# Kernel optimization log

Measured on AMD Instinct MI355X. Metric: run time of the kernel, lower is better.

The kernel has to match this reference:

```python
import jax, jax.numpy as jnp
import numpy as np

B, T, NODE, IN_CH = 4, 8192, 64, 3
F, L, OUT, H = 256, 10, 48, 4
SFI_LAYER = (1, 3, 5, 7)
S = len(SFI_LAYER)
ALPHA = 1.0
EPS = 1e-5


def setup_inputs():
    ks = iter(jax.random.split(jax.random.key(0), 40))
    def nrm(shape, s=0.02):
        return jax.random.normal(next(ks), shape, jnp.float32) * s
    return {
        "x": jax.random.normal(next(ks), (B, IN_CH, T, NODE), jnp.float32),
        "mask": jnp.ones((B, 1, T), jnp.float32),
        "conv_in_w": nrm((S + 1, IN_CH)), "conv_in_b": nrm((S + 1,)),
        "conv_t_w": nrm((F, NODE)), "conv_t_b": nrm((F,)),
        "sfi_cs_w": nrm((S, F, NODE)), "sfi_cs_b": nrm((S, F)),
        "sfi_ff1_w": nrm((S, F, F)), "sfi_ff1_b": nrm((S, F)),
        "sfi_ff2_w": nrm((S, F, F)), "sfi_ff2_b": nrm((S, F)),
        "ff_w": nrm((L, F, F, 3)), "ff_b": nrm((L, F)),
        "qw": nrm((L, F, F)), "qb": nrm((L, F)),
        "kw": nrm((L, F, F)), "kb": nrm((L, F)),
        "vw": nrm((L, F, F)), "vb": nrm((L, F)),
        "ow": nrm((L, F, F)), "ob": nrm((L, F)),
        "co_w": nrm((L, F, F)), "co_b": nrm((L, F)),
        "out_w": nrm((OUT, F)), "out_b": nrm((OUT,)),
    }


def _dconv1d(x, w, b, dilation):
    # x: [B,C,T], w: [O,I,3]; 'same' length via padding=dilation
    y = jax.lax.conv_general_dilated(
        x, w, window_strides=(1,), padding=[(dilation, dilation)],
        rhs_dilation=(dilation,), dimension_numbers=("NCH", "OIH", "NCH"))
    return y + b[None, :, None]


def _inorm(x):
    # InstanceNorm1d, affine=False: normalize each (b,c) over T, biased var
    m = x.mean(-1, keepdims=True)
    v = x.var(-1, keepdims=True)
    return (x - m) * jax.lax.rsqrt(v + EPS)


def _lin_att(q, wq, bq, wk, bk, wv, bv, wo, bo, mask):
    # q: [B,L,C]; sigmoid-kernelized linear attention
    Bn, Ln, C = q.shape
    d = C // H
    def heads(w, b):
        return (q @ w.T + b).reshape(Bn, Ln, H, d).transpose(0, 2, 1, 3)
    Q = jax.nn.sigmoid(heads(wq, bq))  # [B,H,L,d]
    K = jax.nn.sigmoid(heads(wk, bk))
    V = heads(wv, bv)
    KV = jnp.einsum("bhsd,bhse->bhde", K, V)               # [B,H,d,d]
    Z = 1.0 / jnp.einsum("bhld,bhd->bhl", Q, K.sum(2) + 1e-6)
    o = jnp.einsum("bhde,bhld,bhl->bhle", KV, Q, Z)         # [B,H,L,d]
    o = o.transpose(0, 2, 1, 3).reshape(Bn, Ln, C) @ wo.T + bo
    return o * mask[:, 0, :, None]


def _sfi(fs, ft, csw, csb, f1w, f1b, f2w, f2b, mask):
    # fs: [B,T,node], ft: [B,F,T]
    fsc = jnp.einsum("btn,fn->bft", fs, csw) + csb[None, :, None]
    attn = jax.nn.softmax(jnp.einsum("bct,bdt->bcd", fsc, ft) / ft.shape[-1], axis=-1)
    cross = jnp.einsum("bcd,bdt->bct", attn, ft) + ft
    h = cross.transpose(0, 2, 1)                           # [B,T,F]
    h = jax.nn.gelu(h @ f1w.T + f1b, approximate=False) @ f2w.T + f2b
    return (h.transpose(0, 2, 1) + ft) * mask


def _att_module(x, ffw, ffb, wq, bq, wk, bk, wv, bv, wo, bo, cow, cob, mask, dilation):
    out = jax.nn.relu(_dconv1d(x, ffw, ffb, dilation))
    qn = _inorm(out).transpose(0, 2, 1)                    # [B,T,F]
    out = ALPHA * _lin_att(qn, wq, bq, wk, bk, wv, bv, wo, bo, mask).transpose(0, 2, 1) + out
    out = jnp.einsum("bct,oc->bot", out, cow) + cob[None, :, None]
    return (x + out) * mask


def reference(x, mask, conv_in_w, conv_in_b, conv_t_w, conv_t_b,
              sfi_cs_w, sfi_cs_b, sfi_ff1_w, sfi_ff1_b, sfi_ff2_w, sfi_ff2_b,
              ff_w, ff_b, qw, qb, kw, kb, vw, vb, ow, ob, co_w, co_b,
              out_w, out_b):
    # eval mode: all dropouts are identity
    xi = jnp.einsum("bitn,oi->botn", x, conv_in_w) + conv_in_b[None, :, None, None]
    feature_s = xi[:, :S]                                  # [B,S,T,node]
    ft = xi[:, S].transpose(0, 2, 1)                       # [B,node,T]
    fst = jnp.einsum("bnt,fn->bft", ft, conv_t_w) + conv_t_b[None, :, None]
    count = 0
    for i in range(L):
        if i in SFI_LAYER:
            fst = _sfi(feature_s[:, count], fst,
                       sfi_cs_w[count], sfi_cs_b[count],
                       sfi_ff1_w[count], sfi_ff1_b[count],
                       sfi_ff2_w[count], sfi_ff2_b[count], mask)
            count += 1
        fst = _att_module(fst, ff_w[i], ff_b[i], qw[i], qb[i], kw[i], kb[i],
                          vw[i], vb[i], ow[i], ob[i], co_w[i], co_b[i], mask, 2 ** i)
    out = jnp.einsum("bct,oc->bot", fst, out_w) + out_b[None, :, None]
    return out * mask
```

## Files before the change

kernel.cpp:

```cpp
#include <hip/hip_runtime.h>

#define T_ 8192
#define B_ 4

typedef _Float16 h16;
typedef _Float16 half8 __attribute__((ext_vector_type(8)));
typedef float    f32x4 __attribute__((ext_vector_type(4)));

__device__ __forceinline__ void split2(float v, h16* hp, h16* lp) {
  h16 h = (h16)v; *hp = h; *lp = (h16)(v - (float)h);
}
__device__ __forceinline__ float join2(h16 h, h16 l) {
  return (float)h + (float)l;
}
__device__ __forceinline__ void gl2lds16(const void* g, void* l) {
  __builtin_amdgcn_global_load_lds(
      (const __attribute__((address_space(1))) unsigned int*)g,
      (__attribute__((address_space(3))) unsigned int*)l, 16, 0, 0);
}

__global__ __launch_bounds__(256) void init_fs_k(
    const float* __restrict__ x, const float* __restrict__ cw,
    const float* __restrict__ cb, h16* __restrict__ sh, h16* __restrict__ sl,
    int c)
{
  size_t idx = (size_t)blockIdx.x * 256 + threadIdx.x;
  int n = (int)(idx & 63);
  int t = (int)((idx >> 6) & (T_ - 1));
  int b = (int)(idx >> 19);
  float x0 = x[(((size_t)b*3 + 0)*T_ + t)*64 + n];
  float x1 = x[(((size_t)b*3 + 1)*T_ + t)*64 + n];
  float x2 = x[(((size_t)b*3 + 2)*T_ + t)*64 + n];
  float v = cb[c] + x0*cw[c*3] + x1*cw[c*3+1] + x2*cw[c*3+2];
  split2(v, &sh[idx], &sl[idx]);
}

__global__ __launch_bounds__(256) void wsplit_k(
    const float* __restrict__ src, h16* __restrict__ dh, h16* __restrict__ dl,
    int n)
{
  int i = blockIdx.x*256 + threadIdx.x;
  if (i < n) split2(src[i], &dh[i], &dl[i]);
}

__global__ __launch_bounds__(256) void wsplit_out_k(
    const float* __restrict__ src, h16* __restrict__ dh, h16* __restrict__ dl)
{
  int i = blockIdx.x*256 + threadIdx.x;
  int row = i >> 8;
  float v = (row < 48) ? src[i] : 0.f;
  split2(v, &dh[i], &dl[i]);
}

__global__ __launch_bounds__(256) void prep_layer_k(
    const float* __restrict__ ffw, const float* __restrict__ cow,
    const float* __restrict__ ow, const float* __restrict__ ob,
    const float* __restrict__ cob,
    h16* __restrict__ dh,
    float* __restrict__ bias3, float* __restrict__ stats)
{
  int blk = blockIdx.x, tid = threadIdx.x;
  if (blk < 1024) {
    int i = blk*256 + tid;
    if (i < 196608) {
      int tap = i >> 16, nk = i & 65535;
      dh[i] = (h16)ffw[(size_t)nk*3 + tap];
    } else {
      int e = i - 196608;
      int n = e >> 8, k = e & 255;
      dh[196608 + n*512 + 256 + k] = (h16)cow[e];
    }
  } else if (blk < 1280) {
    int n = blk - 1024;
    __shared__ float Ar[256];
    int k = tid;
    Ar[k] = cow[n*256 + k];
    __syncthreads();
    float acc = 0.f;
    #pragma unroll 4
    for (int j = 0; j < 256; ++j) acc = fmaf(Ar[j], ow[j*256 + k], acc);
    dh[196608 + n*512 + k] = (h16)acc;
  } else if (blk == 1280) {
    int n = tid;
    float s = cob[n];
    #pragma unroll 4
    for (int j = 0; j < 256; ++j) s = fmaf(cow[n*256 + j], ob[j], s);
    bias3[n] = s;
  } else {
    stats[(blk - 1281)*256 + tid] = 0.f;
  }
}

__global__ __launch_bounds__(256) void sprep_k(
    const float* __restrict__ f1, const float* __restrict__ f2,
    const float* __restrict__ cs, h16* __restrict__ dh, h16* __restrict__ dl)
{
  int i = blockIdx.x*256 + threadIdx.x;
  float v = (i < 65536) ? f1[i] : (i < 131072) ? f2[i-65536] : cs[i-131072];
  split2(v, &dh[i], &dl[i]);
}

__global__ __launch_bounds__(256) void nwnb_k(
    const float* __restrict__ qw, const float* __restrict__ kw,
    const float* __restrict__ vw,
    const float* __restrict__ qb, const float* __restrict__ kb,
    const float* __restrict__ vb,
    const float* __restrict__ stats,
    h16* __restrict__ dh, float* __restrict__ bias2)
{
  int blk = blockIdx.x, tid = threadIdx.x;
  if (blk < 3072) {
    int i = blk*256 + tid;
    int k = i & 255;
    int b = (i >> 16) & 3;
    int sel = i >> 18;
    float sm = stats[b*512 + k] * (1.f/T_);
    float s2 = stats[b*512 + 256 + k] * (1.f/T_);
    float iv = rsqrtf(fmaxf(s2 - sm*sm, 0.f) + 1e-5f);
    const float* w = sel == 0 ? kw : sel == 1 ? vw : qw;
    dh[i] = (h16)(w[i & 65535] * iv);
  } else {
    int base = (blk - 3072) * 4;
    int g = tid >> 6, l = tid & 63;
    int id = base + g;
    int n = id & 255, b = (id >> 8) & 3, sel = id >> 10;
    const float* w  = sel == 0 ? kw : sel == 1 ? vw : qw;
    const float* bb = sel == 0 ? kb : sel == 1 ? vb : qb;
    float s = 0.f;
    #pragma unroll
    for (int j = 0; j < 4; ++j) {
      int k = l*4 + j;
      float sm = stats[b*512 + k] * (1.f/T_);
      float s2 = stats[b*512 + 256 + k] * (1.f/T_);
      float iv = rsqrtf(fmaxf(s2 - sm*sm, 0.f) + 1e-5f);
      s += sm * iv * w[n*256 + k];
    }
    #pragma unroll
    for (int off = 32; off > 0; off >>= 1) s += __shfl_xor(s, off);
    if (l == 0) bias2[id] = bb[n] - s;
  }
}

__global__ __launch_bounds__(256) void mmrow_k(
    const float* __restrict__ A, const float* __restrict__ Bm,
    h16* __restrict__ dh)
{
  int n  = blockIdx.x & 255;
  int bb = blockIdx.x >> 8;
  __shared__ float Ar[256];
  int k = threadIdx.x;
  Ar[k] = A[n*256 + k];
  __syncthreads();
  const float* Bb = Bm + (size_t)bb*65536;
  float acc = 0.f;
  #pragma unroll 4
  for (int j = 0; j < 256; ++j) acc = fmaf(Ar[j], Bb[j*256 + k], acc);
  acc += Ar[k];
  dh[(size_t)bb*65536 + (size_t)n*256 + k] = (h16)acc;
}

template<int ACT, int SGL>
__global__ __launch_bounds__(256, 2) void gemm_p(
    const h16* __restrict__ Agh, const h16* __restrict__ Agl,
    const h16* __restrict__ Wgh, const h16* __restrict__ Wgl,
    const float* __restrict__ bias,
    const h16* __restrict__ Rh, const h16* __restrict__ Rl,
    h16* __restrict__ Ch, h16* __restrict__ Cl,
    int K, size_t wbs)
{
  int b  = blockIdx.z;
  int n0 = blockIdx.x * 128;
  int t0 = blockIdx.y * 128;
  const h16* Ah_g = Agh + (size_t)b*T_*K;
  const h16* Al_g = Agl + (size_t)b*T_*K;
  const h16* Wh_g = Wgh + (size_t)b*wbs;
  const h16* Wl_g = Wgl + (size_t)b*wbs;
  __shared__ h16 S[16384];
  int tid = threadIdx.x, l = tid & 63, wid = tid >> 6;
  int wr = wid >> 1, wc = wid & 1, lr = l & 15, kg = l >> 4;
  f32x4 acc[4][4];
  #pragma unroll
  for (int m = 0; m < 4; ++m)
    #pragma unroll
    for (int n = 0; n < 4; ++n) acc[m][n] = (f32x4){0.f,0.f,0.f,0.f};

  for (int k0 = 0; k0 < K; k0 += 32) {
    #pragma unroll
    for (int i = 0; i < 8; ++i) {
      int c = i*256 + tid;
      int p = c >> 9, r = (c >> 2) & 127, kc = c & 3;
      int ks = k0 + ((kc ^ ((r >> 1) & 3)) << 3);
      const h16* src = (p == 0) ? Ah_g + (size_t)(t0 + r)*K + ks
                     : (p == 1) ? Al_g + (size_t)(t0 + r)*K + ks
                     : (p == 2) ? Wh_g + (size_t)(n0 + r)*K + ks
                                : Wl_g + (size_t)(n0 + r)*K + ks;
      gl2lds16(src, S + (size_t)c*8);
    }
    __syncthreads();
    half8 ah[4], al[4], wh[4], wl[4];
    #pragma unroll
    for (int m = 0; m < 4; ++m) {
      int row = wr*64 + m*16 + lr;
      int ko = (kg ^ ((row >> 1) & 3)) * 8;
      ah[m] = *(const half8*)&S[row*32 + ko];
      al[m] = *(const half8*)&S[4096 + row*32 + ko];
    }
    #pragma unroll
    for (int n = 0; n < 4; ++n) {
      int row = wc*64 + n*16 + lr;
      int ko = (kg ^ ((row >> 1) & 3)) * 8;
      wh[n] = *(const half8*)&S[8192 + row*32 + ko];
      wl[n] = *(const half8*)&S[12288 + row*32 + ko];
    }
    #pragma unroll
    for (int m = 0; m < 4; ++m)
      #pragma unroll
      for (int n = 0; n < 4; ++n) {
        acc[m][n] = __builtin_amdgcn_mfma_f32_16x16x32_f16(ah[m], wh[n], acc[m][n], 0, 0, 0);
        acc[m][n] = __builtin_amdgcn_mfma_f32_16x16x32_f16(al[m], wh[n], acc[m][n], 0, 0, 0);
        acc[m][n] = __builtin_amdgcn_mfma_f32_16x16x32_f16(ah[m], wl[n], acc[m][n], 0, 0, 0);
      }
    __syncthreads();
  }
  float* Sf = (float*)S;
  const int LS = 132;
  int erow = tid >> 3;
  int ecol = (tid & 7) * 16;
  #pragma unroll
  for (int m = 0; m < 4; ++m) {
    int lr0 = wr*16 + kg*4;
    #pragma unroll
    for (int n = 0; n < 4; ++n) {
      int lcol = wc*64 + n*16 + lr;
      Sf[(lr0+0)*LS + lcol] = acc[m][n][0];
      Sf[(lr0+1)*LS + lcol] = acc[m][n][1];
      Sf[(lr0+2)*LS + lcol] = acc[m][n][2];
      Sf[(lr0+3)*LS + lcol] = acc[m][n][3];
    }
    __syncthreads();
    int grow = t0 + (erow >> 4)*64 + m*16 + (erow & 15);
    size_t off = ((size_t)b*T_ + grow)*256 + n0 + ecol;
    float f[16];
    #pragma unroll
    for (int j = 0; j < 16; ++j) f[j] = Sf[erow*LS + ecol + j];
    #pragma unroll
    for (int j = 0; j < 16; ++j) {
      float v = f[j];
      if (bias) v += bias[n0 + ecol + j];
      if (ACT == 1) v = fmaxf(v, 0.f);
      if (ACT == 2) v = 1.f/(1.f + __expf(-v));
      if (ACT == 3) v = 0.5f*v*(1.f + erff(v*0.7071067811865475f));
      f[j] = v;
    }
    if (Rh) {
      half8 rh0 = *(const half8*)(Rh + off), rh1 = *(const half8*)(Rh + off + 8);
      half8 rl0 = *(const half8*)(Rl + off), rl1 = *(const half8*)(Rl + off + 8);
      #pragma unroll
      for (int j = 0; j < 8; ++j) { f[j] += join2(rh0[j], rl0[j]); f[j+8] += join2(rh1[j], rl1[j]); }
    }
    if (SGL) {
      half8 o0, o1;
      #pragma unroll
      for (int j = 0; j < 8; ++j) { o0[j] = (h16)f[j]; o1[j] = (h16)f[j+8]; }
      *(half8*)(Ch + off) = o0; *(half8*)(Ch + off + 8) = o1;
    } else {
      half8 oh0, ol0, oh1, ol1;
      #pragma unroll
      for (int j = 0; j < 8; ++j) {
        h16 hh = (h16)f[j];   oh0[j] = hh; ol0[j] = (h16)(f[j]   - (float)hh);
        h16 h2 = (h16)f[j+8]; oh1[j] = h2; ol1[j] = (h16)(f[j+8] - (float)h2);
      }
      *(half8*)(Ch + off) = oh0; *(half8*)(Ch + off + 8) = oh1;
      *(half8*)(Cl + off) = ol0; *(half8*)(Cl + off + 8) = ol1;
    }
    __syncthreads();
  }
}

template<int ACT>
__global__ __launch_bounds__(256, 2) void gemm_p_wh(
    const h16* __restrict__ Agh, const h16* __restrict__ Agl,
    const h16* __restrict__ Wg,
    const float* __restrict__ bias,
    const h16* __restrict__ Rh, const h16* __restrict__ Rl,
    h16* __restrict__ Ch, h16* __restrict__ Cl,
    size_t wbs)
{
  int b  = blockIdx.z;
  int n0 = blockIdx.x * 128;
  int t0 = blockIdx.y * 128;
  const h16* Ah_g = Agh + (size_t)b*T_*256;
  const h16* Al_g = Agl + (size_t)b*T_*256;
  const h16* W_g  = Wg + (size_t)b*wbs;
  __shared__ h16 S[24576];
  int tid = threadIdx.x, l = tid & 63, wid = tid >> 6;
  int wr = wid >> 1, wc = wid & 1, lr = l & 15, kg = l >> 4;
  f32x4 acc[4][4];
  #pragma unroll
  for (int m = 0; m < 4; ++m)
    #pragma unroll
    for (int n = 0; n < 4; ++n) acc[m][n] = (f32x4){0.f,0.f,0.f,0.f};

  for (int k0 = 0; k0 < 256; k0 += 64) {
    #pragma unroll
    for (int i = 0; i < 12; ++i) {
      int c = i*256 + tid;
      int p = c >> 9, r = (c >> 2) & 127, kc = c & 3;
      int ks = k0 + (p & 1)*32 + ((kc ^ ((r >> 1) & 3)) << 3);
      const h16* src = (p < 2) ? Ah_g + (size_t)(t0 + r)*256 + ks
                     : (p < 4) ? Al_g + (size_t)(t0 + r)*256 + ks
                               : W_g  + (size_t)(n0 + r)*256 + ks;
      gl2lds16(src, S + (size_t)c*8);
    }
    __syncthreads();
    half8 a0[4], a1[4], l0[4], l1[4], w0[4], w1[4];
    #pragma unroll
    for (int m = 0; m < 4; ++m) {
      int row = wr*64 + m*16 + lr;
      int ko = (kg ^ ((row >> 1) & 3)) * 8;
      a0[m] = *(const half8*)&S[row*32 + ko];
      a1[m] = *(const half8*)&S[4096 + row*32 + ko];
      l0[m] = *(const half8*)&S[8192 + row*32 + ko];
      l1[m] = *(const half8*)&S[12288 + row*32 + ko];
    }
    #pragma unroll
    for (int n = 0; n < 4; ++n) {
      int row = wc*64 + n*16 + lr;
      int ko = (kg ^ ((row >> 1) & 3)) * 8;
      w0[n] = *(const half8*)&S[16384 + row*32 + ko];
      w1[n] = *(const half8*)&S[20480 + row*32 + ko];
    }
    #pragma unroll
    for (int m = 0; m < 4; ++m)
      #pragma unroll
      for (int n = 0; n < 4; ++n) {
        acc[m][n] = __builtin_amdgcn_mfma_f32_16x16x32_f16(a0[m], w0[n], acc[m][n], 0, 0, 0);
        acc[m][n] = __builtin_amdgcn_mfma_f32_16x16x32_f16(l0[m], w0[n], acc[m][n], 0, 0, 0);
        acc[m][n] = __builtin_amdgcn_mfma_f32_16x16x32_f16(a1[m], w1[n], acc[m][n], 0, 0, 0);
        acc[m][n] = __builtin_amdgcn_mfma_f32_16x16x32_f16(l1[m], w1[n], acc[m][n], 0, 0, 0);
      }
    __syncthreads();
  }
  float* Sf = (float*)S;
  const int LS = 132;
  int erow = tid >> 3;
  int ecol = (tid & 7) * 16;
  #pragma unroll
  for (int m = 0; m < 4; ++m) {
    int lr0 = wr*16 + kg*4;
    #pragma unroll
    for (int n = 0; n < 4; ++n) {
      int lcol = wc*64 + n*16 + lr;
      Sf[(lr0+0)*LS + lcol] = acc[m][n][0];
      Sf[(lr0+1)*LS + lcol] = acc[m][n][1];
      Sf[(lr0+2)*LS + lcol] = acc[m][n][2];
      Sf[(lr0+3)*LS + lcol] = acc[m][n][3];
    }
    __syncthreads();
    int grow = t0 + (erow >> 4)*64 + m*16 + (erow & 15);
    size_t off = ((size_t)b*T_ + grow)*256 + n0 + ecol;
    float f[16];
    #pragma unroll
    for (int j = 0; j < 16; ++j) {
      float v = Sf[erow*LS + ecol + j] + bias[n0 + ecol + j];
      if (ACT == 3) v = 0.5f*v*(1.f + erff(v*0.7071067811865475f));
      f[j] = v;
    }
    if (Rh) {
      half8 rh0 = *(const half8*)(Rh + off), rh1 = *(const half8*)(Rh + off + 8);
      half8 rl0 = *(const half8*)(Rl + off), rl1 = *(const half8*)(Rl + off + 8);
      #pragma unroll
      for (int j = 0; j < 8; ++j) { f[j] += join2(rh0[j], rl0[j]); f[j+8] += join2(rh1[j], rl1[j]); }
    }
    half8 oh0, ol0, oh1, ol1;
    #pragma unroll
    for (int j = 0; j < 8; ++j) {
      h16 hh = (h16)f[j];   oh0[j] = hh; ol0[j] = (h16)(f[j]   - (float)hh);
      h16 h2 = (h16)f[j+8]; oh1[j] = h2; ol1[j] = (h16)(f[j+8] - (float)h2);
    }
    *(half8*)(Ch + off) = oh0; *(half8*)(Ch + off + 8) = oh1;
    *(half8*)(Cl + off) = ol0; *(half8*)(Cl + off + 8) = ol1;
    __syncthreads();
  }
}

__global__ __launch_bounds__(256, 2) void gemm_attout(
    const h16* __restrict__ A1f, const h16* __restrict__ A2f,
    const h16* __restrict__ Wg,
    const float* __restrict__ bias,
    const h16* __restrict__ Rh, const h16* __restrict__ Rl,
    h16* __restrict__ Ch, h16* __restrict__ Cl)
{
  int b  = blockIdx.z;
  int n0 = blockIdx.x * 128;
  int t0 = blockIdx.y * 128;
  size_t abase = (size_t)b*T_*256;
  __shared__ h16 S[16384];
  int tid = threadIdx.x, l = tid & 63, wid = tid >> 6;
  int wr = wid >> 1, wc = wid & 1, lr = l & 15, kg = l >> 4;
  f32x4 acc[4][4];
  #pragma unroll
  for (int m = 0; m < 4; ++m)
    #pragma unroll
    for (int n = 0; n < 4; ++n) acc[m][n] = (f32x4){0.f,0.f,0.f,0.f};

  for (int k0 = 0; k0 < 512; k0 += 64) {
    #pragma unroll
    for (int i = 0; i < 8; ++i) {
      int c = i*256 + tid;
      int p = c >> 9, r = (c >> 2) & 127, kc = c & 3;
      int ks = k0 + (p & 1)*32 + ((kc ^ ((r >> 1) & 3)) << 3);
      const h16* src;
      if (p < 2) {
        if (ks < 256) src = A1f + abase + (size_t)(t0 + r)*256 + ks;
        else          src = A2f + abase + (size_t)(t0 + r)*256 + (ks - 256);
      } else {
        src = Wg + (size_t)(n0 + r)*512 + ks;
      }
      gl2lds16(src, S + (size_t)c*8);
    }
    __syncthreads();
    half8 a0[4], a1[4], w0[4], w1[4];
    #pragma unroll
    for (int m = 0; m < 4; ++m) {
      int row = wr*64 + m*16 + lr;
      int ko = (kg ^ ((row >> 1) & 3)) * 8;
      a0[m] = *(const half8*)&S[row*32 + ko];
      a1[m] = *(const half8*)&S[4096 + row*32 + ko];
    }
    #pragma unroll
    for (int n = 0; n < 4; ++n) {
      int row = wc*64 + n*16 + lr;
      int ko = (kg ^ ((row >> 1) & 3)) * 8;
      w0[n] = *(const half8*)&S[8192 + row*32 + ko];
      w1[n] = *(const half8*)&S[12288 + row*32 + ko];
    }
    #pragma unroll
    for (int m = 0; m < 4; ++m)
      #pragma unroll
      for (int n = 0; n < 4; ++n) {
        acc[m][n] = __builtin_amdgcn_mfma_f32_16x16x32_f16(a0[m], w0[n], acc[m][n], 0, 0, 0);
        acc[m][n] = __builtin_amdgcn_mfma_f32_16x16x32_f16(a1[m], w1[n], acc[m][n], 0, 0, 0);
      }
    __syncthreads();
  }
  float* Sf = (float*)S;
  const int LS = 132;
  int erow = tid >> 3;
  int ecol = (tid & 7) * 16;
  #pragma unroll
  for (int m = 0; m < 4; ++m) {
    int lr0 = wr*16 + kg*4;
    #pragma unroll
    for (int n = 0; n < 4; ++n) {
      int lcol = wc*64 + n*16 + lr;
      Sf[(lr0+0)*LS + lcol] = acc[m][n][0];
      Sf[(lr0+1)*LS + lcol] = acc[m][n][1];
      Sf[(lr0+2)*LS + lcol] = acc[m][n][2];
      Sf[(lr0+3)*LS + lcol] = acc[m][n][3];
    }
    __syncthreads();
    int grow = t0 + (erow >> 4)*64 + m*16 + (erow & 15);
    size_t off = ((size_t)b*T_ + grow)*256 + n0 + ecol;
    float f[16];
    #pragma unroll
    for (int j = 0; j < 16; ++j) f[j] = Sf[erow*LS + ecol + j] + bias[n0 + ecol + j];
    half8 rh0 = *(const half8*)(Rh + off), rh1 = *(const half8*)(Rh + off + 8);
    half8 rl0 = *(const half8*)(Rl + off), rl1 = *(const half8*)(Rl + off + 8);
    #pragma unroll
    for (int j = 0; j < 8; ++j) { f[j] += join2(rh0[j], rl0[j]); f[j+8] += join2(rh1[j], rl1[j]); }
    half8 oh0, ol0, oh1, ol1;
    #pragma unroll
    for (int j = 0; j < 8; ++j) {
      h16 hh = (h16)f[j];   oh0[j] = hh; ol0[j] = (h16)(f[j]   - (float)hh);
      h16 h2 = (h16)f[j+8]; oh1[j] = h2; ol1[j] = (h16)(f[j+8] - (float)h2);
    }
    *(half8*)(Ch + off) = oh0; *(half8*)(Ch + off + 8) = oh1;
    *(half8*)(Cl + off) = ol0; *(half8*)(Cl + off + 8) = ol1;
    __syncthreads();
  }
}

__global__ __launch_bounds__(256, 2) void gemm_qkv(
    const h16* __restrict__ Af, const h16* __restrict__ Wqkv,
    const float* __restrict__ bias2,
    h16* __restrict__ Kf, h16* __restrict__ Vf, h16* __restrict__ Qf)
{
  int fid = blockIdx.x;
  int swz = (fid & 7)*192 + (fid >> 3);
  int xsel = swz % 6;
  int sel = xsel >> 1;
  int n0  = (xsel & 1) * 128;
  int t0  = ((swz / 6) & 63) * 128;
  int b   = swz / 384;
  const h16* A_g = Af + (size_t)b*T_*256;
  const h16* W_g = Wqkv + (size_t)(sel*4 + b)*65536;
  const float* bias = bias2 + (size_t)(sel*4 + b)*256;
  h16* dst = sel == 0 ? Kf : sel == 1 ? Vf : Qf;
  __shared__ h16 S[16384];
  int tid = threadIdx.x, l = tid & 63, wid = tid >> 6;
  int wr = wid >> 1, wc = wid & 1, lr = l & 15, kg = l >> 4;
  f32x4 acc[4][4];
  #pragma unroll
  for (int m = 0; m < 4; ++m)
    #pragma unroll
    for (int n = 0; n < 4; ++n) acc[m][n] = (f32x4){0.f,0.f,0.f,0.f};

  for (int k0 = 0; k0 < 256; k0 += 64) {
    #pragma unroll
    for (int i = 0; i < 8; ++i) {
      int c = i*256 + tid;
      int p = c >> 9, r = (c >> 2) & 127, kc = c & 3;
      int ks = k0 + (p & 1)*32 + ((kc ^ ((r >> 1) & 3)) << 3);
      const h16* src = (p < 2) ? A_g + (size_t)(t0 + r)*256 + ks
                               : W_g + (size_t)(n0 + r)*256 + ks;
      gl2lds16(src, S + (size_t)c*8);
    }
    __syncthreads();
    half8 a0[4], a1[4], w0[4], w1[4];
    #pragma unroll
    for (int m = 0; m < 4; ++m) {
      int row = wr*64 + m*16 + lr;
      int ko = (kg ^ ((row >> 1) & 3)) * 8;
      a0[m] = *(const half8*)&S[row*32 + ko];
      a1[m] = *(const half8*)&S[4096 + row*32 + ko];
    }
    #pragma unroll
    for (int n = 0; n < 4; ++n) {
      int row = wc*64 + n*16 + lr;
      int ko = (kg ^ ((row >> 1) & 3)) * 8;
      w0[n] = *(const half8*)&S[8192 + row*32 + ko];
      w1[n] = *(const half8*)&S[12288 + row*32 + ko];
    }
    #pragma unroll
    for (int m = 0; m < 4; ++m)
      #pragma unroll
      for (int n = 0; n < 4; ++n) {
        acc[m][n] = __builtin_amdgcn_mfma_f32_16x16x32_f16(a0[m], w0[n], acc[m][n], 0, 0, 0);
        acc[m][n] = __builtin_amdgcn_mfma_f32_16x16x32_f16(a1[m], w1[n], acc[m][n], 0, 0, 0);
      }
    __syncthreads();
  }
  float* Sf = (float*)S;
  const int LS = 132;
  int erow = tid >> 3;
  int ecol = (tid & 7) * 16;
  #pragma unroll
  for (int m = 0; m < 4; ++m) {
    int lr0 = wr*16 + kg*4;
    #pragma unroll
    for (int n = 0; n < 4; ++n) {
      int lcol = wc*64 + n*16 + lr;
      Sf[(lr0+0)*LS + lcol] = acc[m][n][0];
      Sf[(lr0+1)*LS + lcol] = acc[m][n][1];
      Sf[(lr0+2)*LS + lcol] = acc[m][n][2];
      Sf[(lr0+3)*LS + lcol] = acc[m][n][3];
    }
    __syncthreads();
    int grow = t0 + (erow >> 4)*64 + m*16 + (erow & 15);
    size_t off = ((size_t)b*T_ + grow)*256 + n0 + ecol;
    half8 o0, o1;
    #pragma unroll
    for (int j = 0; j < 8; ++j) {
      float v0 = Sf[erow*LS + ecol + j]     + bias[n0 + ecol + j];
      float v1 = Sf[erow*LS + ecol + 8 + j] + bias[n0 + ecol + 8 + j];
      if (sel != 1) {
        v0 = 1.f/(1.f + __expf(-v0));
        v1 = 1.f/(1.f + __expf(-v1));
      }
      o0[j] = (h16)v0; o1[j] = (h16)v1;
    }
    *(half8*)(dst + off) = o0; *(half8*)(dst + off + 8) = o1;
    __syncthreads();
  }
}

__global__ __launch_bounds__(256, 2) void conv_p(
    const h16* __restrict__ Agh,
    const h16* __restrict__ Wg,
    const float* __restrict__ bias,
    h16* __restrict__ Cf,
    float* __restrict__ stats, const float* __restrict__ zbuf, int dil)
{
  int fid = blockIdx.x;
  int swz = (fid & 7)*64 + (fid >> 3);
  int n0 = (swz & 1) * 128;
  int t0 = ((swz >> 1) & 63) * 128;
  int b  = swz >> 7;
  const h16* Ah_g = Agh + (size_t)b*T_*256;
  __shared__ h16 S[16384];
  __shared__ float cstat[2][128];
  int tid = threadIdx.x, l = tid & 63, wid = tid >> 6;
  int wr = wid >> 1, wc = wid & 1, lr = l & 15, kg = l >> 4;
  f32x4 acc[4][4];
  #pragma unroll
  for (int m = 0; m < 4; ++m)
    #pragma unroll
    for (int n = 0; n < 4; ++n) acc[m][n] = (f32x4){0.f,0.f,0.f,0.f};

  for (int tap = 0; tap < 3; ++tap) {
    int off = (tap - 1) * dil;
    const h16* W_t = Wg + (size_t)tap*65536;
    for (int k0 = 0; k0 < 256; k0 += 64) {
      #pragma unroll
      for (int i = 0; i < 8; ++i) {
        int c = i*256 + tid;
        int p = c >> 9, r = (c >> 2) & 127, kc = c & 3;
        int ks = k0 + (p & 1)*32 + ((kc ^ ((r >> 1) & 3)) << 3);
        const h16* src;
        if (p < 2) {
          int rt = t0 + r + off;
          if ((unsigned)rt < (unsigned)T_)
            src = Ah_g + (size_t)rt*256 + ks;
          else
            src = (const h16*)zbuf;
        } else {
          src = W_t + (size_t)(n0 + r)*256 + ks;
        }
        gl2lds16(src, S + (size_t)c*8);
      }
      __syncthreads();
      half8 a0[4], a1[4], w0[4], w1[4];
      #pragma unroll
      for (int m = 0; m < 4; ++m) {
        int row = wr*64 + m*16 + lr;
        int ko = (kg ^ ((row >> 1) & 3)) * 8;
        a0[m] = *(const half8*)&S[row*32 + ko];
        a1[m] = *(const half8*)&S[4096 + row*32 + ko];
      }
      #pragma unroll
      for (int n = 0; n < 4; ++n) {
        int row = wc*64 + n*16 + lr;
        int ko = (kg ^ ((row >> 1) & 3)) * 8;
        w0[n] = *(const half8*)&S[8192 + row*32 + ko];
        w1[n] = *(const half8*)&S[12288 + row*32 + ko];
      }
      #pragma unroll
      for (int m = 0; m < 4; ++m)
        #pragma unroll
        for (int n = 0; n < 4; ++n) {
          acc[m][n] = __builtin_amdgcn_mfma_f32_16x16x32_f16(a0[m], w0[n], acc[m][n], 0, 0, 0);
          acc[m][n] = __builtin_amdgcn_mfma_f32_16x16x32_f16(a1[m], w1[n], acc[m][n], 0, 0, 0);
        }
      __syncthreads();
    }
  }
  cstat[tid >> 7][tid & 127] = 0.f;
  __syncthreads();
  #pragma unroll
  for (int n = 0; n < 4; ++n) {
    int cl = wc*64 + n*16 + lr;
    float bi = bias[n0 + cl];
    float s = 0.f, s2 = 0.f;
    #pragma unroll
    for (int m = 0; m < 4; ++m)
      #pragma unroll
      for (int r = 0; r < 4; ++r) {
        float v = fmaxf(acc[m][n][r] + bi, 0.f);
        acc[m][n][r] = v;
        s += v; s2 += v*v;
      }
    atomicAdd(&cstat[0][cl], s);
    atomicAdd(&cstat[1][cl], s2);
  }
  __syncthreads();
  if (tid < 128)      atomicAdd(&stats[b*512 + n0 + tid], cstat[0][tid]);
  else if (tid < 256) atomicAdd(&stats[b*512 + 256 + n0 + (tid-128)], cstat[1][tid-128]);
  __syncthreads();
  float* Sf = (float*)S;
  const int LS = 132;
  int erow = tid >> 3;
  int ecol = (tid & 7) * 16;
  #pragma unroll
  for (int m = 0; m < 4; ++m) {
    int lr0 = wr*16 + kg*4;
    #pragma unroll
    for (int n = 0; n < 4; ++n) {
      int lcol = wc*64 + n*16 + lr;
      Sf[(lr0+0)*LS + lcol] = acc[m][n][0];
      Sf[(lr0+1)*LS + lcol] = acc[m][n][1];
      Sf[(lr0+2)*LS + lcol] = acc[m][n][2];
      Sf[(lr0+3)*LS + lcol] = acc[m][n][3];
    }
    __syncthreads();
    int grow = t0 + (erow >> 4)*64 + m*16 + (erow & 15);
    size_t off2 = ((size_t)b*T_ + grow)*256 + n0 + ecol;
    half8 o0, o1;
    #pragma unroll
    for (int j = 0; j < 8; ++j) {
      o0[j] = (h16)Sf[erow*LS + ecol + j];
      o1[j] = (h16)Sf[erow*LS + ecol + 8 + j];
    }
    *(half8*)(Cf + off2) = o0; *(half8*)(Cf + off2 + 8) = o1;
    __syncthreads();
  }
}

__global__ __launch_bounds__(256) void kv_part_p(
    const h16* __restrict__ Kf, const h16* __restrict__ Vf,
    float* __restrict__ pkv)
{
  int bh = blockIdx.y, b = bh >> 2, h = bh & 3;
  int t0 = blockIdx.x * 512;
  __shared__ h16 S[2][64][64];
  __shared__ float ksum[64];
  int tid = threadIdx.x, l = tid & 63, wid = tid >> 6;
  int lr = l & 15, kg = l >> 4;
  if (tid < 64) ksum[tid] = 0.f;
  float ksp[8] = {};
  f32x4 acc[4];
  #pragma unroll
  for (int n = 0; n < 4; ++n) acc[n] = (f32x4){0.f,0.f,0.f,0.f};

  for (int k0 = 0; k0 < 512; k0 += 64) {
    __syncthreads();
    #pragma unroll
    for (int i = 0; i < 2; ++i) {
      int q = tid + i*256;
      int tt = q >> 3;
      int c8 = (q & 7) * 8;
      size_t row = ((size_t)b*T_ + t0 + k0 + tt)*256 + h*64;
      half8 k8 = *(const half8*)(Kf + row + c8);
      half8 v8 = *(const half8*)(Vf + row + c8);
      int ts = tt ^ ((q & 3) << 3);
      #pragma unroll
      for (int j = 0; j < 8; ++j) {
        S[0][c8+j][ts] = k8[j];
        S[1][c8+j][ts] = v8[j];
        ksp[j] += (float)k8[j];
      }
    }
    __syncthreads();
    half8 a0, a1, b0[4], b1[4];
    {
      int row = wid*16 + lr;
      int ko = (kg*8) ^ (((row >> 3) & 3) << 3);
      a0 = *(const half8*)&S[0][row][ko];
      a1 = *(const half8*)&S[0][row][32 + ko];
    }
    #pragma unroll
    for (int n = 0; n < 4; ++n) {
      int row = n*16 + lr;
      int ko = (kg*8) ^ (((row >> 3) & 3) << 3);
      b0[n] = *(const half8*)&S[1][row][ko];
      b1[n] = *(const half8*)&S[1][row][32 + ko];
    }
    #pragma unroll
    for (int n = 0; n < 4; ++n) {
      acc[n] = __builtin_amdgcn_mfma_f32_16x16x32_f16(a0, b0[n], acc[n], 0, 0, 0);
      acc[n] = __builtin_amdgcn_mfma_f32_16x16x32_f16(a1, b1[n], acc[n], 0, 0, 0);
    }
  }
  __syncthreads();
  {
    int dbase = (tid & 7) * 8;
    #pragma unroll
    for (int j = 0; j < 8; ++j) atomicAdd(&ksum[dbase + j], ksp[j]);
  }
  __syncthreads();
  float* dst = pkv + ((size_t)blockIdx.x*16 + bh)*4160;
  #pragma unroll
  for (int n = 0; n < 4; ++n) {
    int e = n*16 + lr;
    #pragma unroll
    for (int r = 0; r < 4; ++r) {
      int d = wid*16 + kg*4 + r;
      dst[d*64 + e] = acc[n][r];
    }
  }
  if (tid < 64) dst[4096 + tid] = ksum[tid];
}

__global__ __launch_bounds__(256) void kv_final_k(
    const float* __restrict__ pkv, float* __restrict__ kv)
{
  int bh = blockIdx.x;
  for (int idx = threadIdx.x; idx < 4160; idx += 256) {
    float s = 0.f;
    #pragma unroll
    for (int c = 0; c < 16; ++c) s += pkv[((size_t)c*16 + bh)*4160 + idx];
    kv[(size_t)bh*4160 + idx] = s;
  }
}

__global__ __launch_bounds__(256) void att_apply_p(
    const h16* __restrict__ Qf, const float* __restrict__ kv,
    h16* __restrict__ Of)
{
  int bh = blockIdx.y, b = bh >> 2, h = bh & 3;
  int t0 = blockIdx.x * 128;
  __shared__ float QsT[64][132];
  __shared__ float KVs[64][68];
  __shared__ float ks[64];
  int tid = threadIdx.x;
  const float* src = kv + (size_t)bh*4160;
  #pragma unroll
  for (int i = 0; i < 16; ++i) {
    int idx = tid + i*256;
    KVs[idx >> 6][idx & 63] = src[idx];
  }
  if (tid < 64) ks[tid] = src[4096 + tid] + 1e-6f;
  #pragma unroll
  for (int i = 0; i < 4; ++i) {
    int q8 = tid + i*256;
    int t  = q8 >> 3;
    int d8 = (q8 & 7) * 8;
    size_t off = ((size_t)b*T_ + t0 + t)*256 + h*64 + d8;
    half8 qh = *(const half8*)(Qf + off);
    #pragma unroll
    for (int j = 0; j < 8; ++j) QsT[d8+j][t] = (float)qh[j];
  }
  __syncthreads();
  int t2 = (tid >> 2) * 2;
  int e0 = (tid & 3) * 16;
  float acc[2][16] = {};
  float den[2] = {};
  for (int dd = 0; dd < 64; ++dd) {
    float2 q = *(const float2*)&QsT[dd][t2];
    float kd = ks[dd];
    den[0] = fmaf(q.x, kd, den[0]);
    den[1] = fmaf(q.y, kd, den[1]);
    float va[16];
    *(float4*)&va[0]  = *(const float4*)&KVs[dd][e0+0];
    *(float4*)&va[4]  = *(const float4*)&KVs[dd][e0+4];
    *(float4*)&va[8]  = *(const float4*)&KVs[dd][e0+8];
    *(float4*)&va[12] = *(const float4*)&KVs[dd][e0+12];
    #pragma unroll
    for (int j = 0; j < 16; ++j) {
      acc[0][j] = fmaf(q.x, va[j], acc[0][j]);
      acc[1][j] = fmaf(q.y, va[j], acc[1][j]);
    }
  }
  #pragma unroll
  for (int ti = 0; ti < 2; ++ti) {
    float z = 1.f / den[ti];
    size_t off = ((size_t)b*T_ + t0 + t2 + ti)*256 + h*64 + e0;
    half8 v0, v1;
    #pragma unroll
    for (int j = 0; j < 8; ++j) {
      v0[j] = (h16)(acc[ti][j] * z);
      v1[j] = (h16)(acc[ti][j+8] * z);
    }
    *(half8*)(Of + off) = v0;
    *(half8*)(Of + off + 8) = v1;
  }
}

__global__ __launch_bounds__(256, 2) void gram_part_p(
    const h16* __restrict__ Af, const h16* __restrict__ Bf,
    float* __restrict__ pg)
{
  int b = blockIdx.z;
  int quad = blockIdx.y;
  int slab = blockIdx.x;
  int c0 = (quad >> 1) * 128, d0 = (quad & 1) * 128;
  int t0 = slab * 256;
  __shared__ h16 S[2][128][64];
  int tid = threadIdx.x, l = tid & 63, wid = tid >> 6;
  int wr = wid >> 1, wc = wid & 1, lr = l & 15, kg = l >> 4;
  f32x4 acc[4][4];
  #pragma unroll
  for (int m = 0; m < 4; ++m)
    #pragma unroll
    for (int n = 0; n < 4; ++n) acc[m][n] = (f32x4){0.f,0.f,0.f,0.f};

  for (int k0 = 0; k0 < 256; k0 += 64) {
    #pragma unroll
    for (int i = 0; i < 4; ++i) {
      int q = tid + i*256;
      int tt = q >> 4;
      int c8 = (q & 15) * 8;
      size_t row = ((size_t)b*T_ + t0 + k0 + tt) * 256;
      half8 a8 = *(const half8*)(Af + row + c0 + c8);
      half8 b8 = *(const half8*)(Bf + row + d0 + c8);
      int ts = tt ^ ((q & 3) << 3);
      #pragma unroll
      for (int j = 0; j < 8; ++j) {
        S[0][c8+j][ts] = a8[j];
        S[1][c8+j][ts] = b8[j];
      }
    }
    __syncthreads();
    half8 a0[4], a1[4], b0[4], b1[4];
    #pragma unroll
    for (int m = 0; m < 4; ++m) {
      int row = wr*64 + m*16 + lr;
      int ko = (kg*8) ^ (((row >> 3) & 3) << 3);
      a0[m] = *(const half8*)&S[0][row][ko];
      a1[m] = *(const half8*)&S[0][row][32 + ko];
    }
    #pragma unroll
    for (int n = 0; n < 4; ++n) {
      int row = wc*64 + n*16 + lr;
      int ko = (kg*8) ^ (((row >> 3) & 3) << 3);
      b0[n] = *(const half8*)&S[1][row][ko];
      b1[n] = *(const half8*)&S[1][row][32 + ko];
    }
    #pragma unroll
    for (int m = 0; m < 4; ++m)
      #pragma unroll
      for (int n = 0; n < 4; ++n) {
        acc[m][n] = __builtin_amdgcn_mfma_f32_16x16x32_f16(a0[m], b0[n], acc[m][n], 0, 0, 0);
        acc[m][n] = __builtin_amdgcn_mfma_f32_16x16x32_f16(a1[m], b1[n], acc[m][n], 0, 0, 0);
      }
    __syncthreads();
  }
  float* dst = pg + ((size_t)(slab*B_ + b)*4 + quad)*16384;
  #pragma unroll
  for (int m = 0; m < 4; ++m)
    #pragma unroll
    for (int n = 0; n < 4; ++n) {
      int cl = wr*64 + m*16 + kg*4;
      int dl = wc*64 + n*16 + lr;
      #pragma unroll
      for (int r = 0; r < 4; ++r)
        dst[(size_t)(cl + r)*128 + dl] = acc[m][n][r];
    }
}

__global__ __launch_bounds__(64) void gram_smax_p(
    const float* __restrict__ pg, float* __restrict__ G)
{
  int row = blockIdx.x;
  int b = row >> 8, c = row & 255;
  int l = threadIdx.x;
  int d4 = l * 4;
  int quad = ((c >= 128) ? 2 : 0) | ((d4 >= 128) ? 1 : 0);
  size_t base = ((size_t)b*4 + quad)*16384 + (size_t)(c & 127)*128 + (d4 & 127);
  float s0 = 0.f, s1 = 0.f, s2 = 0.f, s3 = 0.f;
  for (int sl = 0; sl < 32; ++sl) {
    const float* p = pg + (size_t)sl*(B_*4*16384) + base;
    float4 v = *(const float4*)p;
    s0 += v.x; s1 += v.y; s2 += v.z; s3 += v.w;
  }
  float v[4] = {s0*(1.f/T_), s1*(1.f/T_), s2*(1.f/T_), s3*(1.f/T_)};
  float mx = fmaxf(fmaxf(v[0], v[1]), fmaxf(v[2], v[3]));
  #pragma unroll
  for (int off = 32; off > 0; off >>= 1) mx = fmaxf(mx, __shfl_xor(mx, off));
  float s = 0.f;
  #pragma unroll
  for (int j = 0; j < 4; ++j) { v[j] = __expf(v[j] - mx); s += v[j]; }
  #pragma unroll
  for (int off = 32; off > 0; off >>= 1) s += __shfl_xor(s, off);
  float inv = 1.f / s;
  float4 o = make_float4(v[0]*inv, v[1]*inv, v[2]*inv, v[3]*inv);
  *(float4*)(G + (size_t)b*65536 + (size_t)c*256 + d4) = o;
}

__global__ __launch_bounds__(256, 2) void gemm_out(
    const h16* __restrict__ Agh, const h16* __restrict__ Agl,
    const h16* __restrict__ Wgh, const h16* __restrict__ Wgl,
    const float* __restrict__ bn, const float* __restrict__ mask,
    float* __restrict__ out)
{
  int bt0 = blockIdx.x * 256;
  int b = bt0 >> 13;
  __shared__ h16 S[20480];
  int tid = threadIdx.x, l = tid & 63, wid = tid >> 6;
  int lr = l & 15, kg = l >> 4;
  f32x4 acc[4][4];
  #pragma unroll
  for (int m = 0; m < 4; ++m)
    #pragma unroll
    for (int n = 0; n < 4; ++n) acc[m][n] = (f32x4){0.f,0.f,0.f,0.f};

  for (int k0 = 0; k0 < 256; k0 += 32) {
    #pragma unroll
    for (int i = 0; i < 10; ++i) {
      int c = i*256 + tid;
      const h16* src;
      if (c < 2048) {
        int p = c >> 10, rem = c & 1023, r = rem >> 2, kc = rem & 3;
        int ks = k0 + ((kc ^ ((r >> 1) & 3)) << 3);
        src = (p ? Agl : Agh) + (size_t)(bt0 + r)*256 + ks;
      } else {
        int c2 = c - 2048;
        int p = c2 >> 8, rem = c2 & 255, r = rem >> 2, kc = rem & 3;
        int ks = k0 + ((kc ^ ((r >> 1) & 3)) << 3);
        src = (p ? Wgl : Wgh) + (size_t)r*256 + ks;
      }
      gl2lds16(src, S + (size_t)c*8);
    }
    __syncthreads();
    half8 ah[4], al[4], wh[4], wl[4];
    #pragma unroll
    for (int m = 0; m < 4; ++m) {
      int row = wid*64 + m*16 + lr;
      int ko = ((kg ^ ((row >> 1) & 3)) << 3);
      ah[m] = *(const half8*)&S[row*32 + ko];
      al[m] = *(const half8*)&S[8192 + row*32 + ko];
    }
    #pragma unroll
    for (int n = 0; n < 4; ++n) {
      int row = n*16 + lr;
      int ko = ((kg ^ ((row >> 1) & 3)) << 3);
      wh[n] = *(const half8*)&S[16384 + row*32 + ko];
      wl[n] = *(const half8*)&S[18432 + row*32 + ko];
    }
    #pragma unroll
    for (int m = 0; m < 4; ++m)
      #pragma unroll
      for (int n = 0; n < 4; ++n) {
        acc[m][n] = __builtin_amdgcn_mfma_f32_16x16x32_f16(ah[m], wh[n], acc[m][n], 0, 0, 0);
        acc[m][n] = __builtin_amdgcn_mfma_f32_16x16x32_f16(al[m], wh[n], acc[m][n], 0, 0, 0);
        acc[m][n] = __builtin_amdgcn_mfma_f32_16x16x32_f16(ah[m], wl[n], acc[m][n], 0, 0, 0);
      }
    __syncthreads();
  }
  #pragma unroll
  for (int m = 0; m < 4; ++m)
    #pragma unroll
    for (int n = 0; n < 4; ++n) {
      int col = n*16 + lr;
      if (col < 48) {
        float bi = bn[col];
        #pragma unroll
        for (int r = 0; r < 4; ++r) {
          int grow = bt0 + wid*64 + m*16 + kg*4 + r;
          int t = grow & (T_ - 1);
          out[((size_t)b*48 + col)*T_ + t] =
              (acc[m][n][r] + bi) * mask[(size_t)b*T_ + t];
        }
      }
    }
}

extern "C" void kernel_launch(void* const* d_in, const int* in_sizes, int n_in,
                              void* d_out, int out_size, void* d_ws, size_t ws_size,
                              hipStream_t stream) {
  const float* x         = (const float*)d_in[0];
  const float* mask      = (const float*)d_in[1];
  const float* conv_in_w = (const float*)d_in[2];
  const float* conv_in_b = (const float*)d_in[3];
  const float* conv_t_w  = (const float*)d_in[4];
  const float* conv_t_b  = (const float*)d_in[5];
  const float* sfi_cs_w  = (const float*)d_in[6];
  const float* sfi_cs_b  = (const float*)d_in[7];
  const float* sfi_ff1_w = (const float*)d_in[8];
  const float* sfi_ff1_b = (const float*)d_in[9];
  const float* sfi_ff2_w = (const float*)d_in[10];
  const float* sfi_ff2_b = (const float*)d_in[11];
  const float* ff_w      = (const float*)d_in[12];
  const float* ff_b      = (const float*)d_in[13];
  const float* qw = (const float*)d_in[14]; const float* qb = (const float*)d_in[15];
  const float* kw = (const float*)d_in[16]; const float* kb = (const float*)d_in[17];
  const float* vw = (const float*)d_in[18]; const float* vb = (const float*)d_in[19];
  const float* ow = (const float*)d_in[20]; const float* ob = (const float*)d_in[21];
  const float* co_w = (const float*)d_in[22]; const float* co_b = (const float*)d_in[23];
  const float* out_w = (const float*)d_in[24]; const float* out_b = (const float*)d_in[25];

  float* ws = (float*)d_ws;
  const size_t BT = (size_t)B_ * T_;
  const size_t NB = BT * 256;
  float* smallR = ws;
  float* bigR   = smallR + BT*64;
  float* GR     = bigR + 5*NB;
  float* statsR = GR + (size_t)B_*65536;
  float* kvR    = statsR + (size_t)B_*512;
  float* wsfiR  = kvR + 16*4160;
  float* zbufR  = wsfiR + 147456;

  h16* small_h = (h16*)smallR; h16* small_l = small_h + BT*64;
  h16 *bigH[5], *bigL[5];
  for (int i = 0; i < 5; ++i) { bigH[i] = (h16*)(bigR + (size_t)i*NB); bigL[i] = bigH[i] + NB; }
  float* Gf    = GR;
  float* stats = statsR;
  float* kvbuf = kvR;
  h16* wsfi_h = (h16*)wsfiR; h16* wsfi_l = wsfi_h + 147456;
  float* pkv   = smallR;
  h16* wqkv   = (h16*)smallR;
  h16* wf_h    = (h16*)smallR;
  h16* wlay   = (h16*)(smallR + 1064960);
  float* bias2 = smallR + 1392640;
  float* bias3 = smallR + 1395712;

  dim3 gh(2, T_/128, B_);
  dim3 b256(256);

  hipMemsetAsync(zbufR, 0, 64, stream);
  init_fs_k<<<dim3((unsigned)(BT*64/256)), b256, 0, stream>>>(x, conv_in_w, conv_in_b, small_h, small_l, 4);
  wsplit_k<<<dim3(64), b256, 0, stream>>>(conv_t_w, wsfi_h, wsfi_l, 16384);
  gemm_p<0,0><<<gh, b256, 0, stream>>>(small_h, small_l, wsfi_h, wsfi_l, conv_t_b,
                                       nullptr, nullptr, bigH[0], bigL[0], 64, 0);

  int ifst = 0;
  int fr[4] = {1, 2, 3, 4};
  int count = 0;
  for (int i = 0; i < 10; ++i) {
    if (i == 1 || i == 3 || i == 5 || i == 7) {
      int a = fr[0], bb = fr[1], c = fr[2], d = fr[3];
      sprep_k<<<dim3(576), b256, 0, stream>>>(sfi_ff1_w + (size_t)count*65536,
                                              sfi_ff2_w + (size_t)count*65536,
                                              sfi_cs_w + (size_t)count*16384,
                                              wsfi_h, wsfi_l);
      init_fs_k<<<dim3((unsigned)(BT*64/256)), b256, 0, stream>>>(x, conv_in_w, conv_in_b, small_h, small_l, count);
      gemm_p<0,1><<<gh, b256, 0, stream>>>(small_h, small_l, wsfi_h + 131072, wsfi_l + 131072,
                                           sfi_cs_b + count*256, nullptr, nullptr,
                                           bigH[a], nullptr, 64, 0);
      float* pgram = bigR + (size_t)bb*NB;
      gram_part_p<<<dim3(32, 4, B_), b256, 0, stream>>>(bigH[a], bigH[ifst], pgram);
      gram_smax_p<<<dim3(B_*256), dim3(64), 0, stream>>>(pgram, Gf);
      mmrow_k<<<dim3(B_*256), b256, 0, stream>>>(sfi_ff1_w + (size_t)count*65536, Gf, wf_h);
      gemm_p_wh<3><<<gh, b256, 0, stream>>>(bigH[ifst], bigL[ifst], wf_h,
                                            sfi_ff1_b + count*256, nullptr, nullptr,
                                            bigH[c], bigL[c], 65536);
      gemm_p_wh<0><<<gh, b256, 0, stream>>>(bigH[c], bigL[c], wsfi_h + 65536,
                                            sfi_ff2_b + count*256, bigH[ifst], bigL[ifst],
                                            bigH[d], bigL[d], 0);
      fr[0] = a; fr[1] = bb; fr[2] = c; fr[3] = ifst;
      ifst = d;
      ++count;
    }
    int a = fr[0], bb = fr[1], c = fr[2], d = fr[3];
    int dil = 1 << i;
    prep_layer_k<<<dim3(1289), b256, 0, stream>>>(ff_w + (size_t)i*196608,
                                                  co_w + (size_t)i*65536,
                                                  ow + (size_t)i*65536, ob + i*256,
                                                  co_b + i*256,
                                                  wlay, bias3, stats);
    conv_p<<<dim3(512), b256, 0, stream>>>(bigH[ifst], wlay, ff_b + i*256,
                                           bigH[a], stats, zbufR, dil);
    nwnb_k<<<dim3(3840), b256, 0, stream>>>(qw + (size_t)i*65536, kw + (size_t)i*65536,
                                            vw + (size_t)i*65536,
                                            qb + i*256, kb + i*256, vb + i*256,
                                            stats, wqkv, bias2);
    gemm_qkv<<<dim3(1536), b256, 0, stream>>>(bigH[a], wqkv, bias2,
                                              bigH[bb], bigH[c], bigH[d]);
    kv_part_p<<<dim3(16, 16), b256, 0, stream>>>(bigH[bb], bigH[c], pkv);
    kv_final_k<<<dim3(16), b256, 0, stream>>>(pkv, kvbuf);
    att_apply_p<<<dim3(T_/128, 16), b256, 0, stream>>>(bigH[d], kvbuf, bigH[d]);
    gemm_attout<<<gh, b256, 0, stream>>>(bigH[d], bigH[a],
                                         wlay + 196608, bias3,
                                         bigH[ifst], bigL[ifst], bigH[bb], bigL[bb]);
    fr[0] = a; fr[1] = c; fr[2] = d; fr[3] = ifst;
    ifst = bb;
  }
  wsplit_out_k<<<dim3(64), b256, 0, stream>>>(out_w, wsfi_h, wsfi_l);
  gemm_out<<<dim3((unsigned)(BT/256)), b256, 0, stream>>>(bigH[ifst], bigL[ifst], wsfi_h, wsfi_l,
                                                          out_b, mask, (float*)d_out);
}
```

Baseline: 1.945 ms.

## Move linear-attention apply onto MFMA with split-fp16 transposed KV

The attention-apply step now runs on fp16 MFMA instead of scalar fp32 FMA loops. KV is transposed and stored as hi/lo fp16 pairs, with the key-sum folded in as an extra column so the denominator comes out of the same matrix product. Q and KV tiles are loaded into swizzled LDS through direct global-to-LDS copies. This cuts ALU and LDS work in a kernel that runs every layer, but Q is used only in its fp16 form, and the output stores become scattered 2-byte writes.

```diff
diff --git a/kernel.cpp b/kernel.cpp
--- a/kernel.cpp
+++ b/kernel.cpp
@@ -772,77 +772,104 @@
 }
 
 __global__ __launch_bounds__(256) void kv_final_k(
-    const float* __restrict__ pkv, float* __restrict__ kv)
+    const float* __restrict__ pkv, h16* __restrict__ kvT)
 {
   int bh = blockIdx.x;
-  for (int idx = threadIdx.x; idx < 4160; idx += 256) {
+  for (int idx = threadIdx.x; idx < 5120; idx += 256) {
+    int e = idx >> 6, d = idx & 63;
     float s = 0.f;
-    #pragma unroll
-    for (int c = 0; c < 16; ++c) s += pkv[((size_t)c*16 + bh)*4160 + idx];
-    kv[(size_t)bh*4160 + idx] = s;
+    if (e < 64) {
+      #pragma unroll
+      for (int c = 0; c < 16; ++c) s += pkv[((size_t)c*16 + bh)*4160 + d*64 + e];
+    } else if (e == 64) {
+      #pragma unroll
+      for (int c = 0; c < 16; ++c) s += pkv[((size_t)c*16 + bh)*4160 + 4096 + d];
+      s += 1e-6f;
+    }
+    split2(s, &kvT[(size_t)bh*10240 + idx], &kvT[(size_t)bh*10240 + 5120 + idx]);
   }
 }
 
 __global__ __launch_bounds__(256) void att_apply_p(
-    const h16* __restrict__ Qf, const float* __restrict__ kv,
+    const h16* __restrict__ Qf, const h16* __restrict__ kvT,
     h16* __restrict__ Of)
 {
   int bh = blockIdx.y, b = bh >> 2, h = bh & 3;
   int t0 = blockIdx.x * 128;
-  __shared__ float QsT[64][132];
-  __shared__ float KVs[64][68];
-  __shared__ float ks[64];
-  int tid = threadIdx.x;
-  const float* src = kv + (size_t)bh*4160;
-  #pragma unroll
-  for (int i = 0; i < 16; ++i) {
-    int idx = tid + i*256;
-    KVs[idx >> 6][idx & 63] = src[idx];
-  }
-  if (tid < 64) ks[tid] = src[4096 + tid] + 1e-6f;
+  __shared__ h16 S[18432];
+  int tid = threadIdx.x, l = tid & 63, wid = tid >> 6;
+  int lr = l & 15, kg = l >> 4;
+
   #pragma unroll
   for (int i = 0; i < 4; ++i) {
-    int q8 = tid + i*256;
-    int t  = q8 >> 3;
-    int d8 = (q8 & 7) * 8;
-    size_t off = ((size_t)b*T_ + t0 + t)*256 + h*64 + d8;
-    half8 qh = *(const half8*)(Qf + off);
-    #pragma unroll
-    for (int j = 0; j < 8; ++j) QsT[d8+j][t] = (float)qh[j];
+    int c = i*256 + tid;
+    int r = c >> 3, k8 = c & 7;
+    int half = k8 >> 2, kq = k8 & 3;
+    int kk = (kq ^ ((r >> 1) & 3)) * 8;
+    gl2lds16(Qf + ((size_t)b*T_ + t0 + r)*256 + h*64 + half*32 + kk,
+             S + (size_t)c*8);
+  }
+  const h16* kvb = kvT + (size_t)bh*10240;
+  #pragma unroll
+  for (int i = 0; i < 5; ++i) {
+    int c = i*256 + tid;
+    int p = (c >= 640) ? 1 : 0;
+    int cc = c - p*640;
+    int r = cc >> 3, k8 = cc & 7;
+    int half = k8 >> 2, kq = k8 & 3;
+    int kk = (kq ^ ((r >> 1) & 3)) * 8;
+    gl2lds16(kvb + p*5120 + r*64 + half*32 + kk,
+             S + 8192 + (size_t)c*8);
   }
   __syncthreads();
-  int t2 = (tid >> 2) * 2;
-  int e0 = (tid & 3) * 16;
-  float acc[2][16] = {};
-  float den[2] = {};
-  for (int dd = 0; dd < 64; ++dd) {
-    float2 q = *(const float2*)&QsT[dd][t2];
-    float kd = ks[dd];
-    den[0] = fmaf(q.x, kd, den[0]);
-    den[1] = fmaf(q.y, kd, den[1]);
-    float va[16];
-    *(float4*)&va[0]  = *(const float4*)&KVs[dd][e0+0];
-    *(float4*)&va[4]  = *(const float4*)&KVs[dd][e0+4];
-    *(float4*)&va[8]  = *(const float4*)&KVs[dd][e0+8];
-    *(float4*)&va[12] = *(const float4*)&KVs[dd][e0+12];
-    #pragma unroll
-    for (int j = 0; j < 16; ++j) {
-      acc[0][j] = fmaf(q.x, va[j], acc[0][j]);
-      acc[1][j] = fmaf(q.y, va[j], acc[1][j]);
-    }
-  }
-  #pragma unroll
-  for (int ti = 0; ti < 2; ++ti) {
-    float z = 1.f / den[ti];
-    size_t off = ((size_t)b*T_ + t0 + t2 + ti)*256 + h*64 + e0;
-    half8 v0, v1;
-    #pragma unroll
-    for (int j = 0; j < 8; ++j) {
-      v0[j] = (h16)(acc[ti][j] * z);
-      v1[j] = (h16)(acc[ti][j+8] * z);
-    }
-    *(half8*)(Of + off) = v0;
-    *(half8*)(Of + off + 8) = v1;
+
+  f32x4 acc[2][5];
+  #pragma unroll
+  for (int m = 0; m < 2; ++m)
+    #pragma unroll
+    for (int n = 0; n < 5; ++n) acc[m][n] = (f32x4){0.f,0.f,0.f,0.f};
+
+  half8 a0[2], a1[2];
+  #pragma unroll
+  for (int m = 0; m < 2; ++m) {
+    int row = wid*32 + m*16 + lr;
+    int ko = (kg ^ ((row >> 1) & 3)) * 8;
+    a0[m] = *(const half8*)&S[row*64 + ko];
+    a1[m] = *(const half8*)&S[row*64 + 32 + ko];
+  }
+  #pragma unroll
+  for (int n = 0; n < 5; ++n) {
+    int roww = n*16 + lr;
+    int ko = (kg ^ ((roww >> 1) & 3)) * 8;
+    half8 wh0 = *(const half8*)&S[8192 + roww*64 + ko];
+    half8 wh1 = *(const half8*)&S[8192 + roww*64 + 32 + ko];
+    half8 wl0 = *(const half8*)&S[13312 + roww*64 + ko];
+    half8 wl1 = *(const half8*)&S[13312 + roww*64 + 32 + ko];
+    #pragma unroll
+    for (int m = 0; m < 2; ++m) {
+      acc[m][n] = __builtin_amdgcn_mfma_f32_16x16x32_f16(a0[m], wh0, acc[m][n], 0, 0, 0);
+      acc[m][n] = __builtin_amdgcn_mfma_f32_16x16x32_f16(a0[m], wl0, acc[m][n], 0, 0, 0);
+      acc[m][n] = __builtin_amdgcn_mfma_f32_16x16x32_f16(a1[m], wh1, acc[m][n], 0, 0, 0);
+      acc[m][n] = __builtin_amdgcn_mfma_f32_16x16x32_f16(a1[m], wl1, acc[m][n], 0, 0, 0);
+    }
+  }
+
+  #pragma unroll
+  for (int m = 0; m < 2; ++m) {
+    float z[4];
+    #pragma unroll
+    for (int r = 0; r < 4; ++r) {
+      float dv = __shfl(acc[m][4][r], (l >> 4) << 4);
+      z[r] = 1.f / dv;
+    }
+    #pragma unroll
+    for (int r = 0; r < 4; ++r) {
+      int grow = t0 + wid*32 + m*16 + kg*4 + r;
+      size_t base = ((size_t)b*T_ + grow)*256 + h*64;
+      #pragma unroll
+      for (int n = 0; n < 4; ++n)
+        Of[base + n*16 + lr] = (h16)(acc[m][n][r] * z[r]);
+    }
   }
 }
 
@@ -1057,7 +1084,7 @@
   float* GR     = bigR + 5*NB;
   float* statsR = GR + (size_t)B_*65536;
   float* kvR    = statsR + (size_t)B_*512;
-  float* wsfiR  = kvR + 16*4160;
+  float* wsfiR  = kvR + 81920;
   float* zbufR  = wsfiR + 147456;
 
   h16* small_h = (h16*)smallR; h16* small_l = small_h + BT*64;
@@ -1065,7 +1092,7 @@
   for (int i = 0; i < 5; ++i) { bigH[i] = (h16*)(bigR + (size_t)i*NB); bigL[i] = bigH[i] + NB; }
   float* Gf    = GR;
   float* stats = statsR;
-  float* kvbuf = kvR;
+  h16* kvT16   = (h16*)kvR;
   h16* wsfi_h = (h16*)wsfiR; h16* wsfi_l = wsfi_h + 147456;
   float* pkv   = smallR;
   h16* wqkv   = (h16*)smallR;
@@ -1127,8 +1154,8 @@
     gemm_qkv<<<dim3(1536), b256, 0, stream>>>(bigH[a], wqkv, bias2,
                                               bigH[bb], bigH[c], bigH[d]);
     kv_part_p<<<dim3(16, 16), b256, 0, stream>>>(bigH[bb], bigH[c], pkv);
-    kv_final_k<<<dim3(16), b256, 0, stream>>>(pkv, kvbuf);
-    att_apply_p<<<dim3(T_/128, 16), b256, 0, stream>>>(bigH[d], kvbuf, bigH[d]);
+    kv_final_k<<<dim3(16), b256, 0, stream>>>(pkv, kvT16);
+    att_apply_p<<<dim3(T_/128, 16), b256, 0, stream>>>(bigH[d], kvT16, bigH[d]);
     gemm_attout<<<gh, b256, 0, stream>>>(bigH[d], bigH[a],
                                          wlay + 196608, bias3,
                                          bigH[ifst], bigL[ifst], bigH[bb], bigL[bb]);
```

After: 2.085 ms. +7.2%, slower.
